# Performance work log

Measured on AMD Instinct MI355X. Metric: run time of the kernel, lower is better.

The kernel has to match this reference:

```python
import jax, jax.numpy as jnp
from jax import lax
import numpy as np

KSIZE = 21

def setup_inputs() -> dict:
    key = jax.random.key(0)
    k1, k2 = jax.random.split(key)
    x = jax.random.normal(k1, (32, 3, 512, 512), dtype=jnp.float32)
    kernel = jax.random.uniform(k2, (32, 1, KSIZE, KSIZE), dtype=jnp.float32)
    return {"x": x, "kernel": kernel}

def reference(x, kernel):
    # Per-sample depthwise conv: fuse batch loop into a single grouped conv
    # by folding batch into channels (groups = B*C).
    B, C, H, W = x.shape
    K = kernel.shape[-1]
    pad = K // 2
    # expand the per-sample kernel across channels, shape (B*C, 1, K, K)
    k = jnp.broadcast_to(kernel, (B, C, K, K)).reshape(B * C, 1, K, K)
    xr = x.reshape(1, B * C, H, W)
    out = lax.conv_general_dilated(
        xr, k,
        window_strides=(1, 1),
        padding=[(pad, pad), (pad, pad)],
        dimension_numbers=("NCHW", "OIHW", "NCHW"),
        feature_group_count=B * C,
    )
    return out.reshape(B, C, H, W)
```

## Files before the change

kernel.cpp:

```cpp
#include <hip/hip_runtime.h>

#define KK 21
#define HH 512
#define WW 512
#define CC 3
#define BB 32
#define TILE_Y 64
#define TILE_X 128
#define SROWS 85
#define SSTRIDE 168
#define NKHP 11
#define NB_PER_B (NKHP * 3 * 512)
#define NCHUNK 20
#define NBLK (BB * CC * 32)

typedef __attribute__((ext_vector_type(8))) short short8;
typedef __attribute__((ext_vector_type(4))) float floatx4;

__device__ __forceinline__ unsigned short f2bf(float f) {
    union { float f; unsigned u; } v; v.f = f;
    unsigned r = v.u + 0x7FFF + ((v.u >> 16) & 1);
    return (unsigned short)(r >> 16);
}

__global__ __launch_bounds__(256) void build_B(
    const float* __restrict__ ker, unsigned short* __restrict__ wsB)
{
    const int b = blockIdx.x;
    const float* __restrict__ kp = ker + b * KK * KK;
    unsigned short* __restrict__ wb = wsB + (size_t)b * NB_PER_B;
    for (int e = threadIdx.x; e < NB_PER_B; e += 256) {
        const int j    = e & 7;
        const int n    = (e >> 3) & 15;
        const int q    = (e >> 7) & 3;
        const int f    = e >> 9;
        const int khp  = f / 3;
        const int half = f - khp * 3;
        const int k    = q * 8 + j;
        const int h    = k >> 4;
        const int c    = k & 15;
        const int kh   = 2 * khp + h;
        const int d    = c - n - 2 + 16 * half;
        float v = 0.0f;
        if (kh < KK && d >= 0 && d < KK) v = kp[kh * KK + d];
        wb[e] = f2bf(v);
    }
}

__global__ __launch_bounds__(256, 5) void dwconv_mfma(
    const float* __restrict__ x,
    const unsigned short* __restrict__ wsB,
    float* __restrict__ out)
{
    __shared__ __align__(16) unsigned short s_in[SROWS * SSTRIDE];

    const int rbid = (blockIdx.x & 7) * (NBLK / 8) + (blockIdx.x >> 3);
    const int tiles = (HH / TILE_Y) * (WW / TILE_X);
    const int bc = rbid / tiles;
    const int t  = rbid % tiles;
    const int ty0 = (t / (WW / TILE_X)) * TILE_Y;
    const int tx0 = (t % (WW / TILE_X)) * TILE_X;
    const int b = bc / CC;

    const float* __restrict__ xp = x + (size_t)bc * HH * WW;
    const unsigned short* __restrict__ wsb = wsB + (size_t)b * NB_PER_B;
    const int tid = threadIdx.x;

    for (int i = tid; i < SROWS * NCHUNK; i += 256) {
        const int ly  = i / NCHUNK;
        const int k   = i - ly * NCHUNK;
        const int gy  = ty0 - 10 + ly;
        const int gx0 = tx0 - 12 + 8 * k;
        float4 v0 = make_float4(0.f, 0.f, 0.f, 0.f);
        float4 v1 = make_float4(0.f, 0.f, 0.f, 0.f);
        if (gy >= 0 && gy < HH) {
            const float* __restrict__ rp = xp + (size_t)gy * WW;
            if (gx0 >= 0 && gx0 + 7 < WW) {
                v0 = *(const float4*)(rp + gx0);
                v1 = *(const float4*)(rp + gx0 + 4);
            } else {
                if (gx0 + 0 >= 0 && gx0 + 0 < WW) v0.x = rp[gx0 + 0];
                if (gx0 + 1 >= 0 && gx0 + 1 < WW) v0.y = rp[gx0 + 1];
                if (gx0 + 2 >= 0 && gx0 + 2 < WW) v0.z = rp[gx0 + 2];
                if (gx0 + 3 >= 0 && gx0 + 3 < WW) v0.w = rp[gx0 + 3];
                if (gx0 + 4 >= 0 && gx0 + 4 < WW) v1.x = rp[gx0 + 4];
                if (gx0 + 5 >= 0 && gx0 + 5 < WW) v1.y = rp[gx0 + 5];
                if (gx0 + 6 >= 0 && gx0 + 6 < WW) v1.z = rp[gx0 + 6];
                if (gx0 + 7 >= 0 && gx0 + 7 < WW) v1.w = rp[gx0 + 7];
            }
        }
        const int p0 = (int)((unsigned)f2bf(v0.x) | ((unsigned)f2bf(v0.y) << 16));
        const int p1 = (int)((unsigned)f2bf(v0.z) | ((unsigned)f2bf(v0.w) << 16));
        const int p2 = (int)((unsigned)f2bf(v1.x) | ((unsigned)f2bf(v1.y) << 16));
        const int p3 = (int)((unsigned)f2bf(v1.z) | ((unsigned)f2bf(v1.w) << 16));
        *(int4*)&s_in[ly * SSTRIDE + 8 * k] = make_int4(p0, p1, p2, p3);
    }
    __syncthreads();

    const int lane = tid & 63;
    const int wv   = tid >> 6;
    const int mrow = lane & 15;
    const int qd   = lane >> 4;

    floatx4 acc[8];
#pragma unroll
    for (int tt = 0; tt < 8; ++tt) acc[tt] = (floatx4){0.f, 0.f, 0.f, 0.f};

    const unsigned short* bbase = wsb + lane * 8;
    const unsigned short* abase = s_in + ((16 * wv + mrow + (qd >> 1)) * SSTRIDE) + 8 * (qd & 1);

    short8 nb1 = *(const short8*)(bbase);
    short8 nb2 = *(const short8*)(bbase + 512);
    short8 nb3 = *(const short8*)(bbase + 1024);

#pragma unroll 1
    for (int khp = 0; khp < NKHP; ++khp) {
        const short8 b1 = nb1;
        const short8 b2 = nb2;
        const short8 b3 = nb3;
        const int khn = (khp < NKHP - 1) ? (khp + 1) : khp;
        nb1 = *(const short8*)(bbase + khn * 1536);
        nb2 = *(const short8*)(bbase + khn * 1536 + 512);
        nb3 = *(const short8*)(bbase + khn * 1536 + 1024);

        const unsigned short* arow = abase + 2 * khp * SSTRIDE;
        short8 a[10];
#pragma unroll
        for (int s = 0; s < 10; ++s) a[s] = *(const short8*)(arow + 16 * s);

#pragma unroll
        for (int tt = 0; tt < 8; ++tt) {
            acc[tt] = __builtin_amdgcn_mfma_f32_16x16x32_bf16(a[tt],     b1, acc[tt], 0, 0, 0);
            acc[tt] = __builtin_amdgcn_mfma_f32_16x16x32_bf16(a[tt + 1], b2, acc[tt], 0, 0, 0);
            acc[tt] = __builtin_amdgcn_mfma_f32_16x16x32_bf16(a[tt + 2], b3, acc[tt], 0, 0, 0);
        }
    }

    float* __restrict__ op = out + (size_t)bc * HH * WW;
#pragma unroll
    for (int tt = 0; tt < 8; ++tt) {
#pragma unroll
        for (int r = 0; r < 4; ++r) {
            const int y = ty0 + 16 * wv + qd * 4 + r;
            const int xcol = tx0 + 16 * tt + mrow;
            op[(size_t)y * WW + xcol] = acc[tt][r];
        }
    }
}

extern "C" void kernel_launch(void* const* d_in, const int* in_sizes, int n_in,
                              void* d_out, int out_size, void* d_ws, size_t ws_size,
                              hipStream_t stream) {
    const float* x   = (const float*)d_in[0];
    const float* ker = (const float*)d_in[1];
    float* out = (float*)d_out;
    unsigned short* wsB = (unsigned short*)d_ws;

    build_B<<<BB, 256, 0, stream>>>(ker, wsB);

    dwconv_mfma<<<NBLK, 256, 0, stream>>>(x, wsB, out);
}
```

Measured before the change: 218.4 us.

## Pre-pad and convert input to bf16, then DMA tiles directly into LDS

```diff
diff --git a/kernel.cpp b/kernel.cpp
--- a/kernel.cpp
+++ b/kernel.cpp
@@ -5,14 +5,26 @@
 #define WW 512
 #define CC 3
 #define BB 32
+#define NBC (BB * CC)
 #define TILE_Y 64
 #define TILE_X 128
 #define SROWS 85
 #define SSTRIDE 168
 #define NKHP 11
 #define NB_PER_B (NKHP * 3 * 512)
-#define NCHUNK 20
-#define NBLK (BB * CC * 32)
+#define NBLK (NBC * 32)
+
+#define PW 560
+#define PH 533
+#define PCHUNK 70
+#define PAD_PER_BC ((size_t)PH * PW)
+#define CPB (PH * PCHUNK)
+#define PADBLK_PER_BC 146
+#define B_ELEMS ((size_t)BB * NB_PER_B)
+#define B_BYTES (B_ELEMS * 2)
+#define WS_NEED (B_BYTES + (size_t)NBC * PAD_PER_BC * 2)
+#define NDMA (SROWS * 21)
+#define NCHUNK_FB 20
 
 typedef __attribute__((ext_vector_type(8))) short short8;
 typedef __attribute__((ext_vector_type(4))) float floatx4;
@@ -21,6 +33,12 @@
     union { float f; unsigned u; } v; v.f = f;
     unsigned r = v.u + 0x7FFF + ((v.u >> 16) & 1);
     return (unsigned short)(r >> 16);
+}
+
+__device__ __forceinline__ void dma16(const unsigned short* g, unsigned short* l) {
+    __builtin_amdgcn_global_load_lds(
+        (const __attribute__((address_space(1))) unsigned int*)g,
+        (__attribute__((address_space(3))) unsigned int*)l, 16, 0, 0);
 }
 
 __global__ __launch_bounds__(256) void build_B(
@@ -47,28 +65,137 @@
     }
 }
 
+__global__ __launch_bounds__(256) void pad_bf16(
+    const float* __restrict__ x, unsigned short* __restrict__ px)
+{
+    const int bc = blockIdx.x / PADBLK_PER_BC;
+    const int i  = (blockIdx.x % PADBLK_PER_BC) * 256 + threadIdx.x;
+    if (i >= CPB) return;
+    const int r   = i / PCHUNK;
+    const int c   = i - r * PCHUNK;
+    const int gy  = r - 10;
+    const int gx0 = 8 * c - 12;
+    float4 v0 = make_float4(0.f, 0.f, 0.f, 0.f);
+    float4 v1 = make_float4(0.f, 0.f, 0.f, 0.f);
+    if (gy >= 0 && gy < HH) {
+        const float* __restrict__ rp = x + (size_t)bc * HH * WW + (size_t)gy * WW;
+        if (gx0 >= 0 && gx0 + 7 < WW) {
+            v0 = *(const float4*)(rp + gx0);
+            v1 = *(const float4*)(rp + gx0 + 4);
+        } else {
+            if (gx0 + 0 >= 0 && gx0 + 0 < WW) v0.x = rp[gx0 + 0];
+            if (gx0 + 1 >= 0 && gx0 + 1 < WW) v0.y = rp[gx0 + 1];
+            if (gx0 + 2 >= 0 && gx0 + 2 < WW) v0.z = rp[gx0 + 2];
+            if (gx0 + 3 >= 0 && gx0 + 3 < WW) v0.w = rp[gx0 + 3];
+            if (gx0 + 4 >= 0 && gx0 + 4 < WW) v1.x = rp[gx0 + 4];
+            if (gx0 + 5 >= 0 && gx0 + 5 < WW) v1.y = rp[gx0 + 5];
+            if (gx0 + 6 >= 0 && gx0 + 6 < WW) v1.z = rp[gx0 + 6];
+            if (gx0 + 7 >= 0 && gx0 + 7 < WW) v1.w = rp[gx0 + 7];
+        }
+    }
+    const int p0 = (int)((unsigned)f2bf(v0.x) | ((unsigned)f2bf(v0.y) << 16));
+    const int p1 = (int)((unsigned)f2bf(v0.z) | ((unsigned)f2bf(v0.w) << 16));
+    const int p2 = (int)((unsigned)f2bf(v1.x) | ((unsigned)f2bf(v1.y) << 16));
+    const int p3 = (int)((unsigned)f2bf(v1.z) | ((unsigned)f2bf(v1.w) << 16));
+    *(int4*)(px + (size_t)bc * PAD_PER_BC + (size_t)r * PW + 8 * c) = make_int4(p0, p1, p2, p3);
+}
+
 __global__ __launch_bounds__(256, 5) void dwconv_mfma(
+    const unsigned short* __restrict__ px,
+    const unsigned short* __restrict__ wsB,
+    float* __restrict__ out)
+{
+    __shared__ __align__(16) unsigned short s_in[SROWS * SSTRIDE];
+
+    const int bc  = blockIdx.x >> 5;
+    const int t   = blockIdx.x & 31;
+    const int ty0 = (t >> 2) * TILE_Y;
+    const int tx0 = (t & 3) * TILE_X;
+    const int b   = bc / CC;
+    const int tid = threadIdx.x;
+
+    const unsigned short* __restrict__ pb =
+        px + (size_t)bc * PAD_PER_BC + (size_t)ty0 * PW + tx0;
+#pragma unroll
+    for (int k = 0; k < 7; ++k) {
+        const int i = tid + 256 * k;
+        if (k < 6 || i < NDMA) {
+            const int ly = i / 21;
+            const int c  = i - ly * 21;
+            dma16(pb + (size_t)ly * PW + 8 * c, s_in + 8 * i);
+        }
+    }
+    __syncthreads();
+
+    const int lane = tid & 63;
+    const int wv   = tid >> 6;
+    const int mrow = lane & 15;
+    const int qd   = lane >> 4;
+
+    floatx4 acc[8];
+#pragma unroll
+    for (int tt = 0; tt < 8; ++tt) acc[tt] = (floatx4){0.f, 0.f, 0.f, 0.f};
+
+    const unsigned short* bbase = wsB + (size_t)b * NB_PER_B + lane * 8;
+    const unsigned short* abase = s_in + ((16 * wv + mrow + (qd >> 1)) * SSTRIDE) + 8 * (qd & 1);
+
+    short8 nb1 = *(const short8*)(bbase);
+    short8 nb2 = *(const short8*)(bbase + 512);
+    short8 nb3 = *(const short8*)(bbase + 1024);
+
+#pragma unroll 1
+    for (int khp = 0; khp < NKHP; ++khp) {
+        const short8 b1 = nb1;
+        const short8 b2 = nb2;
+        const short8 b3 = nb3;
+        const int khn = (khp < NKHP - 1) ? (khp + 1) : khp;
+        nb1 = *(const short8*)(bbase + khn * 1536);
+        nb2 = *(const short8*)(bbase + khn * 1536 + 512);
+        nb3 = *(const short8*)(bbase + khn * 1536 + 1024);
+
+        const unsigned short* arow = abase + 2 * khp * SSTRIDE;
+        short8 a[10];
+#pragma unroll
+        for (int s = 0; s < 10; ++s) a[s] = *(const short8*)(arow + 16 * s);
+
+#pragma unroll
+        for (int tt = 0; tt < 8; ++tt) {
+            acc[tt] = __builtin_amdgcn_mfma_f32_16x16x32_bf16(a[tt],     b1, acc[tt], 0, 0, 0);
+            acc[tt] = __builtin_amdgcn_mfma_f32_16x16x32_bf16(a[tt + 1], b2, acc[tt], 0, 0, 0);
+            acc[tt] = __builtin_amdgcn_mfma_f32_16x16x32_bf16(a[tt + 2], b3, acc[tt], 0, 0, 0);
+        }
+    }
+
+    float* __restrict__ op = out + (size_t)bc * HH * WW;
+#pragma unroll
+    for (int tt = 0; tt < 8; ++tt) {
+#pragma unroll
+        for (int r = 0; r < 4; ++r) {
+            const int y = ty0 + 16 * wv + qd * 4 + r;
+            const int xcol = tx0 + 16 * tt + mrow;
+            op[(size_t)y * WW + xcol] = acc[tt][r];
+        }
+    }
+}
+
+__global__ __launch_bounds__(256, 5) void dwconv_mfma_fb(
     const float* __restrict__ x,
     const unsigned short* __restrict__ wsB,
     float* __restrict__ out)
 {
     __shared__ __align__(16) unsigned short s_in[SROWS * SSTRIDE];
 
-    const int rbid = (blockIdx.x & 7) * (NBLK / 8) + (blockIdx.x >> 3);
-    const int tiles = (HH / TILE_Y) * (WW / TILE_X);
-    const int bc = rbid / tiles;
-    const int t  = rbid % tiles;
-    const int ty0 = (t / (WW / TILE_X)) * TILE_Y;
-    const int tx0 = (t % (WW / TILE_X)) * TILE_X;
-    const int b = bc / CC;
-
+    const int bc  = blockIdx.x >> 5;
+    const int t   = blockIdx.x & 31;
+    const int ty0 = (t >> 2) * TILE_Y;
+    const int tx0 = (t & 3) * TILE_X;
+    const int b   = bc / CC;
     const float* __restrict__ xp = x + (size_t)bc * HH * WW;
-    const unsigned short* __restrict__ wsb = wsB + (size_t)b * NB_PER_B;
     const int tid = threadIdx.x;
 
-    for (int i = tid; i < SROWS * NCHUNK; i += 256) {
-        const int ly  = i / NCHUNK;
-        const int k   = i - ly * NCHUNK;
+    for (int i = tid; i < SROWS * NCHUNK_FB; i += 256) {
+        const int ly  = i / NCHUNK_FB;
+        const int k   = i - ly * NCHUNK_FB;
         const int gy  = ty0 - 10 + ly;
         const int gx0 = tx0 - 12 + 8 * k;
         float4 v0 = make_float4(0.f, 0.f, 0.f, 0.f);
@@ -106,7 +233,7 @@
 #pragma unroll
     for (int tt = 0; tt < 8; ++tt) acc[tt] = (floatx4){0.f, 0.f, 0.f, 0.f};
 
-    const unsigned short* bbase = wsb + lane * 8;
+    const unsigned short* bbase = wsB + (size_t)b * NB_PER_B + lane * 8;
     const unsigned short* abase = s_in + ((16 * wv + mrow + (qd >> 1)) * SSTRIDE) + 8 * (qd & 1);
 
     short8 nb1 = *(const short8*)(bbase);
@@ -158,5 +285,11 @@
 
     build_B<<<BB, 256, 0, stream>>>(ker, wsB);
 
-    dwconv_mfma<<<NBLK, 256, 0, stream>>>(x, wsB, out);
-}
+    if (ws_size >= WS_NEED) {
+        unsigned short* px = wsB + B_ELEMS;
+        pad_bf16<<<NBC * PADBLK_PER_BC, 256, 0, stream>>>(x, px);
+        dwconv_mfma<<<NBLK, 256, 0, stream>>>(px, wsB, out);
+    } else {
+        dwconv_mfma_fb<<<NBLK, 256, 0, stream>>>(x, wsB, out);
+    }
+}
```

After: 240.3 us. 1.1x slower.
